# Optimization experiments

Measured on AMD Instinct MI355X. Metric: run time of the kernel, lower is better.

Reference implementation:

```python
import jax, jax.numpy as jnp
import numpy as np

NEG_INF = -1e30  # stands in for float('-inf'); sigmoid(-1e30)==0 in fp32


def _safe_l2_normalize(x):
    # norm over last dim; norms equal to 0 are replaced by 1 (torch masked_fill_)
    n = jnp.linalg.norm(x, axis=-1, keepdims=True)
    return x / jnp.where(n == 0, 1.0, n)


def setup_inputs() -> dict:
    key = jax.random.key(0)
    k1, k2, k3 = jax.random.split(key, 3)
    B, S, D = 32, 1024, 512
    context = jax.random.normal(k1, (B, S, D), dtype=jnp.float32)
    query = jax.random.normal(k2, (B, S, D), dtype=jnp.float32)
    length = jax.random.randint(k3, (B,), 1, S + 1, dtype=jnp.int64)
    return {"context": context, "query": query, "length": length}


def reference(context, query, length):
    # context: [B, Sc, D], query: [B, Sq, D], length: [B]
    B, Sq, D = query.shape
    Sc = context.shape[1]

    q = _safe_l2_normalize(query)          # normalize=True path
    context_key = _safe_l2_normalize(context)

    # raw bilinear scores [B, Sq, Sc]
    raw_scores = jnp.einsum('bqd,bkd->bqk', q, context_key)

    # mask context positions >= length[b] with -inf (per-sample length mask)
    key_mask = jnp.arange(Sc)[None, None, :] < length[:, None, None]
    raw_scores = jnp.where(key_mask, raw_scores, NEG_INF)

    scores = jax.nn.sigmoid(raw_scores)

    # L1-normalize along context dim; norms < 1 replaced by 1
    scores_norm = jnp.sum(jnp.abs(scores), axis=2, keepdims=True)
    scores = scores / jnp.where(scores_norm < 1, 1.0, scores_norm)

    # zero out query rows >= length[b]
    query_mask = jnp.arange(Sq)[None, :, None] < length[:, None, None]
    scores = jnp.where(query_mask, scores, 0.0)

    attended_context = jnp.einsum('bqk,bkd->bqd', scores, context)
    output = jnp.concatenate([q, attended_context], axis=2)  # [B, Sq, 2D]
    return output, scores
```

## Files before the change

### kernel.cpp

```cpp
#include <hip/hip_runtime.h>
#include <hip/hip_bf16.h>
#include <math.h>

#define BB 32
#define SS 1024
#define DD 512
#define OUT_ELEMS 33554432ull

typedef _Float16 half8 __attribute__((ext_vector_type(8)));
typedef _Float16 half4 __attribute__((ext_vector_type(4)));
typedef float floatx4 __attribute__((ext_vector_type(4)));

__device__ __forceinline__ int load_len(const int* __restrict__ len, int b) {
  const bool is64 = (len[1] == 0);
  return is64 ? (int)((const long long*)len)[b] : len[b];
}

__global__ __launch_bounds__(256) void k_norm(const float* __restrict__ ctx,
                                              const float* __restrict__ qry,
                                              float* __restrict__ out,
                                              float* __restrict__ cinv) {
  const int wid = threadIdx.x >> 6, lane = threadIdx.x & 63;
  const int row = blockIdx.x * 4 + wid;
  const bool isq = row >= BB * SS;
  const int r = isq ? row - BB * SS : row;
  const float4* s4 = (const float4*)((isq ? qry : ctx) + (size_t)r * DD);
  float4 e0 = s4[lane];
  float4 e1 = s4[lane + 64];
  float ss = e0.x*e0.x + e0.y*e0.y + e0.z*e0.z + e0.w*e0.w
           + e1.x*e1.x + e1.y*e1.y + e1.z*e1.z + e1.w*e1.w;
  #pragma unroll
  for (int m = 32; m; m >>= 1) ss += __shfl_xor(ss, m);
  const float inv = (ss > 0.0f) ? (1.0f / sqrtf(ss)) : 1.0f;
  if (isq) {
    float4* dst = (float4*)(out + (size_t)r * (2 * DD));
    float4 o0 = {e0.x*inv, e0.y*inv, e0.z*inv, e0.w*inv};
    float4 o1 = {e1.x*inv, e1.y*inv, e1.z*inv, e1.w*inv};
    dst[lane] = o0;
    dst[lane + 64] = o1;
  } else if (lane == 0) {
    cinv[r] = inv;
  }
}

__global__ __launch_bounds__(256) void k_qk(const float* __restrict__ ctx,
                                            const float* __restrict__ outq,
                                            const float* __restrict__ cinv,
                                            const int* __restrict__ len,
                                            float* __restrict__ sig,
                                            float* __restrict__ denom) {
  __shared__ _Float16 As[128][40];
  __shared__ _Float16 Bs[128][40];
  __shared__ float civ[128];

  const int b = blockIdx.z, bx = blockIdx.x, by = blockIdx.y;
  const int t = threadIdx.x, lane = t & 63, wid = t >> 6;
  const int wm = wid >> 1, wn = wid & 1;
  const int L = load_len(len, b);

  if (t < 128) civ[t] = cinv[b * SS + bx * 128 + t];

  floatx4 acc[4][4] = {};
  const float* qbase = outq + (size_t)(b * SS + by * 128) * (2 * DD);
  const float* cbase = ctx + (size_t)(b * SS + bx * 128) * DD;
  const int rr = lane & 15, g = lane >> 4;

  for (int kt = 0; kt < DD / 32; ++kt) {
    const int k0 = kt * 32;
    __syncthreads();
    #pragma unroll
    for (int it = 0; it < 4; ++it) {
      const int flat = t + it * 256;
      const int r = flat >> 3, cg = flat & 7;
      float4 av = *(const float4*)(qbase + (size_t)r * (2 * DD) + k0 + cg * 4);
      *(half4*)&As[r][cg * 4] =
          (half4){(_Float16)av.x, (_Float16)av.y, (_Float16)av.z, (_Float16)av.w};
      const float ci = civ[r];
      float4 bv = *(const float4*)(cbase + (size_t)r * DD + k0 + cg * 4);
      *(half4*)&Bs[r][cg * 4] =
          (half4){(_Float16)(bv.x * ci), (_Float16)(bv.y * ci),
                  (_Float16)(bv.z * ci), (_Float16)(bv.w * ci)};
    }
    __syncthreads();
    half8 af[4], bf[4];
    #pragma unroll
    for (int i = 0; i < 4; ++i) af[i] = *(const half8*)&As[wm * 64 + i * 16 + rr][g * 8];
    #pragma unroll
    for (int j = 0; j < 4; ++j) bf[j] = *(const half8*)&Bs[wn * 64 + j * 16 + rr][g * 8];
    #pragma unroll
    for (int i = 0; i < 4; ++i)
      #pragma unroll
      for (int j = 0; j < 4; ++j)
        acc[i][j] = __builtin_amdgcn_mfma_f32_16x16x32_f16(af[i], bf[j], acc[i][j], 0, 0, 0);
  }

  const int rowbase = by * 128 + wm * 64, colbase = bx * 128 + wn * 64;
  #pragma unroll
  for (int i = 0; i < 4; ++i) {
    #pragma unroll
    for (int r = 0; r < 4; ++r) {
      const int row = rowbase + i * 16 + g * 4 + r;
      float* srow = sig + (size_t)(b * SS + row) * SS;
      float rsum = 0.0f;
      #pragma unroll
      for (int j = 0; j < 4; ++j) {
        const int col = colbase + j * 16 + rr;
        float v = 0.0f;
        if (col < L) v = 1.0f / (1.0f + __expf(-acc[i][j][r]));
        srow[col] = v;
        rsum += v;
      }
      rsum += __shfl_xor(rsum, 1);
      rsum += __shfl_xor(rsum, 2);
      rsum += __shfl_xor(rsum, 4);
      rsum += __shfl_xor(rsum, 8);
      if (rr == 0) atomicAdd(&denom[b * SS + row], rsum);
    }
  }
}

__global__ __launch_bounds__(512) void k_pv(const float* __restrict__ ctx,
                                            float* __restrict__ sig,
                                            const float* __restrict__ denom,
                                            const int* __restrict__ len,
                                            float* __restrict__ out) {
  __shared__ _Float16 Sh[64][40], Sl[64][40];
  __shared__ _Float16 Ch[512][40], Cl[512][40];
  __shared__ float rds[64];

  const int b = blockIdx.y, bm = blockIdx.x;
  const int t = threadIdx.x, lane = t & 63, wid = t >> 6;
  const int wm = wid >> 2, wn = wid & 3;
  const int rr = lane & 15, g = lane >> 4;
  const int L = load_len(len, b);

  if (t < 64) {
    const int row = bm * 64 + t;
    const float dv = denom[b * SS + row];
    rds[t] = (row < L) ? (1.0f / fmaxf(dv, 1.0f)) : 0.0f;
  }
  __syncthreads();

  floatx4 acc[2][8] = {};
  float* sbase = sig + (size_t)(b * SS + bm * 64) * SS;
  const float* cbase = ctx + (size_t)b * SS * DD;

  const int sr = t >> 3, scg = t & 7;
  const int kg = t & 7, dg = t >> 3;

  for (int kt = 0; kt < SS / 32; ++kt) {
    const int k0 = kt * 32;
    {
      float* sp = sbase + (size_t)sr * SS + k0 + scg * 4;
      float4 v = *(const float4*)sp;
      const float rd = rds[sr];
      float4 nv = {v.x * rd, v.y * rd, v.z * rd, v.w * rd};
      *(float4*)sp = nv;
      _Float16 h0 = (_Float16)v.x, h1 = (_Float16)v.y, h2 = (_Float16)v.z, h3 = (_Float16)v.w;
      *(half4*)&Sh[sr][scg * 4] = (half4){h0, h1, h2, h3};
      *(half4*)&Sl[sr][scg * 4] = (half4){(_Float16)(v.x - (float)h0), (_Float16)(v.y - (float)h1),
                                          (_Float16)(v.z - (float)h2), (_Float16)(v.w - (float)h3)};
    }
    #pragma unroll
    for (int it = 0; it < 2; ++it) {
      const int db = it * 256 + dg * 4;
      const float* cp = cbase + (size_t)(k0 + kg * 4) * DD + db;
      float4 v0 = *(const float4*)(cp);
      float4 v1 = *(const float4*)(cp + DD);
      float4 v2 = *(const float4*)(cp + 2 * DD);
      float4 v3 = *(const float4*)(cp + 3 * DD);
      const float f0[4] = {v0.x, v0.y, v0.z, v0.w};
      const float f1[4] = {v1.x, v1.y, v1.z, v1.w};
      const float f2[4] = {v2.x, v2.y, v2.z, v2.w};
      const float f3[4] = {v3.x, v3.y, v3.z, v3.w};
      #pragma unroll
      for (int i = 0; i < 4; ++i) {
        _Float16 h0 = (_Float16)f0[i], h1 = (_Float16)f1[i], h2 = (_Float16)f2[i], h3 = (_Float16)f3[i];
        *(half4*)&Ch[db + i][kg * 4] = (half4){h0, h1, h2, h3};
        *(half4*)&Cl[db + i][kg * 4] =
            (half4){(_Float16)(f0[i] - (float)h0), (_Float16)(f1[i] - (float)h1),
                    (_Float16)(f2[i] - (float)h2), (_Float16)(f3[i] - (float)h3)};
      }
    }
    __syncthreads();
    half8 sh[2], sl[2];
    #pragma unroll
    for (int i = 0; i < 2; ++i) {
      sh[i] = *(const half8*)&Sh[wm * 32 + i * 16 + rr][g * 8];
      sl[i] = *(const half8*)&Sl[wm * 32 + i * 16 + rr][g * 8];
    }
    #pragma unroll
    for (int j = 0; j < 8; ++j) {
      half8 ch = *(const half8*)&Ch[wn * 128 + j * 16 + rr][g * 8];
      half8 cl = *(const half8*)&Cl[wn * 128 + j * 16 + rr][g * 8];
      #pragma unroll
      for (int i = 0; i < 2; ++i) {
        acc[i][j] = __builtin_amdgcn_mfma_f32_16x16x32_f16(sh[i], ch, acc[i][j], 0, 0, 0);
        acc[i][j] = __builtin_amdgcn_mfma_f32_16x16x32_f16(sh[i], cl, acc[i][j], 0, 0, 0);
        acc[i][j] = __builtin_amdgcn_mfma_f32_16x16x32_f16(sl[i], ch, acc[i][j], 0, 0, 0);
      }
    }
    __syncthreads();
  }

  #pragma unroll
  for (int i = 0; i < 2; ++i) {
    #pragma unroll
    for (int r = 0; r < 4; ++r) {
      const int lrow = wm * 32 + i * 16 + g * 4 + r;
      const int row = bm * 64 + lrow;
      const float rd = rds[lrow];
      float* orow = out + (size_t)(b * SS + row) * (2 * DD) + DD;
      #pragma unroll
      for (int j = 0; j < 8; ++j) {
        const int d = wn * 128 + j * 16 + rr;
        orow[d] = acc[i][j][r] * rd;
      }
    }
  }
}

extern "C" void kernel_launch(void* const* d_in, const int* in_sizes, int n_in,
                              void* d_out, int out_size, void* d_ws, size_t ws_size,
                              hipStream_t stream) {
  const float* ctx = (const float*)d_in[0];
  const float* qry = (const float*)d_in[1];
  const int* len = (const int*)d_in[2];
  float* out = (float*)d_out;
  float* sig = out + OUT_ELEMS;
  float* denom = (float*)d_ws;
  float* cinv = denom + BB * SS;

  hipMemsetAsync(denom, 0, BB * SS * sizeof(float), stream);
  k_norm<<<(2 * BB * SS) / 4, 256, 0, stream>>>(ctx, qry, out, cinv);
  k_qk<<<dim3(SS / 128, SS / 128, BB), 256, 0, stream>>>(ctx, out, cinv, len, sig, denom);
  k_pv<<<dim3(SS / 64, BB), 512, 0, stream>>>(ctx, sig, denom, len, out);
}
```

Measured before the change: 671.7 us.

## Precompute fp16 normalized Q/C in workspace and drop low-half MFMA term in PV

The norm kernel now also writes fp16 copies of the normalized query and context into workspace. A new QK kernel reads these directly with 64-wide K tiles, replacing per-tile fp32 loads and conversion. The fp32 path remains as a fallback when the workspace is too small. The PV kernel drops the context low-part split, going from three MFMAs to two and saving LDS. Both changes cut conversion and memory traffic at the cost of accuracy, since context is now rounded to fp16 in PV.

```diff
diff --git a/kernel.cpp b/kernel.cpp
--- a/kernel.cpp
+++ b/kernel.cpp
@@ -11,6 +11,12 @@
 typedef _Float16 half4 __attribute__((ext_vector_type(4)));
 typedef float floatx4 __attribute__((ext_vector_type(4)));
 
+#define WS_DENOM_OFF   0ull
+#define WS_CINV_OFF    131072ull
+#define WS_QH_OFF      262144ull
+#define WS_CN_OFF      (262144ull + 33554432ull)
+#define WS_NEEDED      (262144ull + 2ull * 33554432ull)
+
 __device__ __forceinline__ int load_len(const int* __restrict__ len, int b) {
   const bool is64 = (len[1] == 0);
   return is64 ? (int)((const long long*)len)[b] : len[b];
@@ -19,7 +25,10 @@
 __global__ __launch_bounds__(256) void k_norm(const float* __restrict__ ctx,
                                               const float* __restrict__ qry,
                                               float* __restrict__ out,
-                                              float* __restrict__ cinv) {
+                                              float* __restrict__ cinv,
+                                              _Float16* __restrict__ qh,
+                                              _Float16* __restrict__ cn,
+                                              int wf) {
   const int wid = threadIdx.x >> 6, lane = threadIdx.x & 63;
   const int row = blockIdx.x * 4 + wid;
   const bool isq = row >= BB * SS;
@@ -32,23 +41,104 @@
   #pragma unroll
   for (int m = 32; m; m >>= 1) ss += __shfl_xor(ss, m);
   const float inv = (ss > 0.0f) ? (1.0f / sqrtf(ss)) : 1.0f;
+  float4 o0 = {e0.x*inv, e0.y*inv, e0.z*inv, e0.w*inv};
+  float4 o1 = {e1.x*inv, e1.y*inv, e1.z*inv, e1.w*inv};
   if (isq) {
     float4* dst = (float4*)(out + (size_t)r * (2 * DD));
-    float4 o0 = {e0.x*inv, e0.y*inv, e0.z*inv, e0.w*inv};
-    float4 o1 = {e1.x*inv, e1.y*inv, e1.z*inv, e1.w*inv};
     dst[lane] = o0;
     dst[lane + 64] = o1;
-  } else if (lane == 0) {
-    cinv[r] = inv;
-  }
-}
-
-__global__ __launch_bounds__(256) void k_qk(const float* __restrict__ ctx,
-                                            const float* __restrict__ outq,
-                                            const float* __restrict__ cinv,
-                                            const int* __restrict__ len,
-                                            float* __restrict__ sig,
-                                            float* __restrict__ denom) {
+    if (wf) {
+      *(half4*)(qh + (size_t)r * DD + 4 * lane) =
+          (half4){(_Float16)o0.x, (_Float16)o0.y, (_Float16)o0.z, (_Float16)o0.w};
+      *(half4*)(qh + (size_t)r * DD + 256 + 4 * lane) =
+          (half4){(_Float16)o1.x, (_Float16)o1.y, (_Float16)o1.z, (_Float16)o1.w};
+    }
+  } else {
+    if (lane == 0) cinv[r] = inv;
+    if (wf) {
+      *(half4*)(cn + (size_t)r * DD + 4 * lane) =
+          (half4){(_Float16)o0.x, (_Float16)o0.y, (_Float16)o0.z, (_Float16)o0.w};
+      *(half4*)(cn + (size_t)r * DD + 256 + 4 * lane) =
+          (half4){(_Float16)o1.x, (_Float16)o1.y, (_Float16)o1.z, (_Float16)o1.w};
+    }
+  }
+}
+
+__global__ __launch_bounds__(256) void k_qk_f16(const _Float16* __restrict__ qh,
+                                                const _Float16* __restrict__ cn,
+                                                const int* __restrict__ len,
+                                                float* __restrict__ sig,
+                                                float* __restrict__ denom) {
+  __shared__ _Float16 As[128][72];
+  __shared__ _Float16 Bs[128][72];
+
+  const int b = blockIdx.z, bx = blockIdx.x, by = blockIdx.y;
+  const int t = threadIdx.x, lane = t & 63, wid = t >> 6;
+  const int wm = wid >> 1, wn = wid & 1;
+  const int L = load_len(len, b);
+  const int rr = lane & 15, g = lane >> 4;
+
+  floatx4 acc[4][4] = {};
+  const _Float16* qbase = qh + (size_t)(b * SS + by * 128) * DD;
+  const _Float16* cbase = cn + (size_t)(b * SS + bx * 128) * DD;
+  const int sr = t >> 3, sc = (t & 7) * 8;
+
+  for (int kt = 0; kt < DD / 64; ++kt) {
+    const int k0 = kt * 64;
+    __syncthreads();
+    #pragma unroll
+    for (int it = 0; it < 4; ++it) {
+      const int r = it * 32 + sr;
+      *(half8*)&As[r][sc] = *(const half8*)(qbase + (size_t)r * DD + k0 + sc);
+      *(half8*)&Bs[r][sc] = *(const half8*)(cbase + (size_t)r * DD + k0 + sc);
+    }
+    __syncthreads();
+    #pragma unroll
+    for (int ks = 0; ks < 2; ++ks) {
+      half8 af[4], bf[4];
+      #pragma unroll
+      for (int i = 0; i < 4; ++i) af[i] = *(const half8*)&As[wm * 64 + i * 16 + rr][ks * 32 + g * 8];
+      #pragma unroll
+      for (int j = 0; j < 4; ++j) bf[j] = *(const half8*)&Bs[wn * 64 + j * 16 + rr][ks * 32 + g * 8];
+      #pragma unroll
+      for (int i = 0; i < 4; ++i)
+        #pragma unroll
+        for (int j = 0; j < 4; ++j)
+          acc[i][j] = __builtin_amdgcn_mfma_f32_16x16x32_f16(af[i], bf[j], acc[i][j], 0, 0, 0);
+    }
+  }
+
+  const int rowbase = by * 128 + wm * 64, colbase = bx * 128 + wn * 64;
+  #pragma unroll
+  for (int i = 0; i < 4; ++i) {
+    #pragma unroll
+    for (int r = 0; r < 4; ++r) {
+      const int row = rowbase + i * 16 + g * 4 + r;
+      float* srow = sig + (size_t)(b * SS + row) * SS;
+      float rsum = 0.0f;
+      #pragma unroll
+      for (int j = 0; j < 4; ++j) {
+        const int col = colbase + j * 16 + rr;
+        float v = 0.0f;
+        if (col < L) v = 1.0f / (1.0f + __expf(-acc[i][j][r]));
+        srow[col] = v;
+        rsum += v;
+      }
+      rsum += __shfl_xor(rsum, 1);
+      rsum += __shfl_xor(rsum, 2);
+      rsum += __shfl_xor(rsum, 4);
+      rsum += __shfl_xor(rsum, 8);
+      if (rr == 0) atomicAdd(&denom[b * SS + row], rsum);
+    }
+  }
+}
+
+__global__ __launch_bounds__(256) void k_qk_fp32(const float* __restrict__ ctx,
+                                                 const float* __restrict__ outq,
+                                                 const float* __restrict__ cinv,
+                                                 const int* __restrict__ len,
+                                                 float* __restrict__ sig,
+                                                 float* __restrict__ denom) {
   __shared__ _Float16 As[128][40];
   __shared__ _Float16 Bs[128][40];
   __shared__ float civ[128];
@@ -125,7 +215,7 @@
                                             const int* __restrict__ len,
                                             float* __restrict__ out) {
   __shared__ _Float16 Sh[64][40], Sl[64][40];
-  __shared__ _Float16 Ch[512][40], Cl[512][40];
+  __shared__ _Float16 Ch[512][40];
   __shared__ float rds[64];
 
   const int b = blockIdx.y, bm = blockIdx.x;
@@ -175,11 +265,8 @@
       const float f3[4] = {v3.x, v3.y, v3.z, v3.w};
       #pragma unroll
       for (int i = 0; i < 4; ++i) {
-        _Float16 h0 = (_Float16)f0[i], h1 = (_Float16)f1[i], h2 = (_Float16)f2[i], h3 = (_Float16)f3[i];
-        *(half4*)&Ch[db + i][kg * 4] = (half4){h0, h1, h2, h3};
-        *(half4*)&Cl[db + i][kg * 4] =
-            (half4){(_Float16)(f0[i] - (float)h0), (_Float16)(f1[i] - (float)h1),
-                    (_Float16)(f2[i] - (float)h2), (_Float16)(f3[i] - (float)h3)};
+        *(half4*)&Ch[db + i][kg * 4] =
+            (half4){(_Float16)f0[i], (_Float16)f1[i], (_Float16)f2[i], (_Float16)f3[i]};
       }
     }
     __syncthreads();
@@ -192,11 +279,9 @@
     #pragma unroll
     for (int j = 0; j < 8; ++j) {
       half8 ch = *(const half8*)&Ch[wn * 128 + j * 16 + rr][g * 8];
-      half8 cl = *(const half8*)&Cl[wn * 128 + j * 16 + rr][g * 8];
       #pragma unroll
       for (int i = 0; i < 2; ++i) {
         acc[i][j] = __builtin_amdgcn_mfma_f32_16x16x32_f16(sh[i], ch, acc[i][j], 0, 0, 0);
-        acc[i][j] = __builtin_amdgcn_mfma_f32_16x16x32_f16(sh[i], cl, acc[i][j], 0, 0, 0);
         acc[i][j] = __builtin_amdgcn_mfma_f32_16x16x32_f16(sl[i], ch, acc[i][j], 0, 0, 0);
       }
     }
@@ -228,11 +313,18 @@
   const int* len = (const int*)d_in[2];
   float* out = (float*)d_out;
   float* sig = out + OUT_ELEMS;
-  float* denom = (float*)d_ws;
-  float* cinv = denom + BB * SS;
+  char* ws = (char*)d_ws;
+  float* denom = (float*)(ws + WS_DENOM_OFF);
+  float* cinv  = (float*)(ws + WS_CINV_OFF);
+  _Float16* qh = (_Float16*)(ws + WS_QH_OFF);
+  _Float16* cn = (_Float16*)(ws + WS_CN_OFF);
+  const int wf = (ws_size >= WS_NEEDED) ? 1 : 0;
 
   hipMemsetAsync(denom, 0, BB * SS * sizeof(float), stream);
-  k_norm<<<(2 * BB * SS) / 4, 256, 0, stream>>>(ctx, qry, out, cinv);
-  k_qk<<<dim3(SS / 128, SS / 128, BB), 256, 0, stream>>>(ctx, out, cinv, len, sig, denom);
+  k_norm<<<(2 * BB * SS) / 4, 256, 0, stream>>>(ctx, qry, out, cinv, qh, cn, wf);
+  if (wf)
+    k_qk_f16<<<dim3(SS / 128, SS / 128, BB), 256, 0, stream>>>(qh, cn, len, sig, denom);
+  else
+    k_qk_fp32<<<dim3(SS / 128, SS / 128, BB), 256, 0, stream>>>(ctx, out, cinv, len, sig, denom);
   k_pv<<<dim3(SS / 64, BB), 512, 0, stream>>>(ctx, sig, denom, len, out);
 }
```

New measurement: 625.1 us. -6.9%, faster.

## Pretranspose context to fp16, load MFMA fragments directly, drop low-part product

Applied to the files above, without the earlier changes.

Adds a transpose kernel that writes context as fp16 [B,D,S] into workspace, so the PV GEMM can load B fragments straight from global memory without LDS staging. The QK GEMM also drops its shared-memory tiles and loads fp32 fragments directly into registers. The PV split-precision scheme drops the context low-part term, cutting MFMAs from three to two per tile. The in-place row scaling of sig moves to after the accumulation loop. The new path depends on workspace size, and the loss of LDS reuse relies on caches to absorb the repeated global loads, which also slightly reduces accuracy.

```diff
diff --git a/kernel.cpp b/kernel.cpp
--- a/kernel.cpp
+++ b/kernel.cpp
@@ -10,6 +10,11 @@
 typedef _Float16 half8 __attribute__((ext_vector_type(8)));
 typedef _Float16 half4 __attribute__((ext_vector_type(4)));
 typedef float floatx4 __attribute__((ext_vector_type(4)));
+
+#define WS_DENOM_OFF 0ull
+#define WS_CINV_OFF  131072ull
+#define WS_CT_OFF    262144ull
+#define WS_NEED_T1   (262144ull + 33554432ull)
 
 __device__ __forceinline__ int load_len(const int* __restrict__ len, int b) {
   const bool is64 = (len[1] == 0);
@@ -33,9 +38,9 @@
   for (int m = 32; m; m >>= 1) ss += __shfl_xor(ss, m);
   const float inv = (ss > 0.0f) ? (1.0f / sqrtf(ss)) : 1.0f;
   if (isq) {
-    float4* dst = (float4*)(out + (size_t)r * (2 * DD));
     float4 o0 = {e0.x*inv, e0.y*inv, e0.z*inv, e0.w*inv};
     float4 o1 = {e1.x*inv, e1.y*inv, e1.z*inv, e1.w*inv};
+    float4* dst = (float4*)(out + (size_t)r * (2 * DD));
     dst[lane] = o0;
     dst[lane + 64] = o1;
   } else if (lane == 0) {
@@ -43,50 +48,69 @@
   }
 }
 
-__global__ __launch_bounds__(256) void k_qk(const float* __restrict__ ctx,
-                                            const float* __restrict__ outq,
-                                            const float* __restrict__ cinv,
-                                            const int* __restrict__ len,
-                                            float* __restrict__ sig,
-                                            float* __restrict__ denom) {
-  __shared__ _Float16 As[128][40];
-  __shared__ _Float16 Bs[128][40];
-  __shared__ float civ[128];
-
+__global__ __launch_bounds__(256) void k_tr(const float* __restrict__ ctx,
+                                            _Float16* __restrict__ ct) {
+  __shared__ _Float16 tile[64][72];
+  const int b = blockIdx.z, dx = blockIdx.y, sx = blockIdx.x;
+  const int t = threadIdx.x;
+  const int s0 = sx * 64, d0 = dx * 64;
+  const int sr = t >> 4, sc = (t & 15) * 4;
+  #pragma unroll
+  for (int it = 0; it < 4; ++it) {
+    const int s = sr + it * 16;
+    float4 v = *(const float4*)(ctx + (size_t)(b * SS + s0 + s) * DD + d0 + sc);
+    tile[sc + 0][s] = (_Float16)v.x;
+    tile[sc + 1][s] = (_Float16)v.y;
+    tile[sc + 2][s] = (_Float16)v.z;
+    tile[sc + 3][s] = (_Float16)v.w;
+  }
+  __syncthreads();
+  const int dr = t >> 2, seg = (t & 3) * 16;
+  _Float16* orow = ct + ((size_t)b * DD + d0 + dr) * SS + s0 + seg;
+  *(half8*)orow = *(const half8*)&tile[dr][seg];
+  *(half8*)(orow + 8) = *(const half8*)&tile[dr][seg + 8];
+}
+
+__global__ __launch_bounds__(256) void k_qk_lf32(const float* __restrict__ ctx,
+                                                 const float* __restrict__ outq,
+                                                 const float* __restrict__ cinv,
+                                                 const int* __restrict__ len,
+                                                 float* __restrict__ sig,
+                                                 float* __restrict__ denom) {
   const int b = blockIdx.z, bx = blockIdx.x, by = blockIdx.y;
   const int t = threadIdx.x, lane = t & 63, wid = t >> 6;
   const int wm = wid >> 1, wn = wid & 1;
+  const int rr = lane & 15, g = lane >> 4;
   const int L = load_len(len, b);
 
-  if (t < 128) civ[t] = cinv[b * SS + bx * 128 + t];
-
   floatx4 acc[4][4] = {};
-  const float* qbase = outq + (size_t)(b * SS + by * 128) * (2 * DD);
-  const float* cbase = ctx + (size_t)(b * SS + bx * 128) * DD;
-  const int rr = lane & 15, g = lane >> 4;
+  const float* abase = outq + (size_t)(b * SS + by * 128 + wm * 64 + rr) * (2 * DD);
+  const int brow0 = b * SS + bx * 128 + wn * 64 + rr;
+  const float* bbase = ctx + (size_t)brow0 * DD;
+  float civ[4];
+  #pragma unroll
+  for (int j = 0; j < 4; ++j) civ[j] = cinv[brow0 + j * 16];
 
   for (int kt = 0; kt < DD / 32; ++kt) {
-    const int k0 = kt * 32;
-    __syncthreads();
-    #pragma unroll
-    for (int it = 0; it < 4; ++it) {
-      const int flat = t + it * 256;
-      const int r = flat >> 3, cg = flat & 7;
-      float4 av = *(const float4*)(qbase + (size_t)r * (2 * DD) + k0 + cg * 4);
-      *(half4*)&As[r][cg * 4] =
-          (half4){(_Float16)av.x, (_Float16)av.y, (_Float16)av.z, (_Float16)av.w};
-      const float ci = civ[r];
-      float4 bv = *(const float4*)(cbase + (size_t)r * DD + k0 + cg * 4);
-      *(half4*)&Bs[r][cg * 4] =
-          (half4){(_Float16)(bv.x * ci), (_Float16)(bv.y * ci),
-                  (_Float16)(bv.z * ci), (_Float16)(bv.w * ci)};
-    }
-    __syncthreads();
+    const int ka = kt * 32 + g * 8;
     half8 af[4], bf[4];
     #pragma unroll
-    for (int i = 0; i < 4; ++i) af[i] = *(const half8*)&As[wm * 64 + i * 16 + rr][g * 8];
-    #pragma unroll
-    for (int j = 0; j < 4; ++j) bf[j] = *(const half8*)&Bs[wn * 64 + j * 16 + rr][g * 8];
+    for (int i = 0; i < 4; ++i) {
+      const float* ap = abase + (size_t)(i * 16) * (2 * DD) + ka;
+      float4 v0 = *(const float4*)ap;
+      float4 v1 = *(const float4*)(ap + 4);
+      af[i] = (half8){(_Float16)v0.x, (_Float16)v0.y, (_Float16)v0.z, (_Float16)v0.w,
+                      (_Float16)v1.x, (_Float16)v1.y, (_Float16)v1.z, (_Float16)v1.w};
+    }
+    #pragma unroll
+    for (int j = 0; j < 4; ++j) {
+      const float* bp = bbase + (size_t)(j * 16) * DD + ka;
+      float4 v0 = *(const float4*)bp;
+      float4 v1 = *(const float4*)(bp + 4);
+      const float c = civ[j];
+      bf[j] = (half8){(_Float16)(v0.x*c), (_Float16)(v0.y*c), (_Float16)(v0.z*c), (_Float16)(v0.w*c),
+                      (_Float16)(v1.x*c), (_Float16)(v1.y*c), (_Float16)(v1.z*c), (_Float16)(v1.w*c)};
+    }
     #pragma unroll
     for (int i = 0; i < 4; ++i)
       #pragma unroll
@@ -119,35 +143,109 @@
   }
 }
 
-__global__ __launch_bounds__(512) void k_pv(const float* __restrict__ ctx,
-                                            float* __restrict__ sig,
-                                            const float* __restrict__ denom,
-                                            const int* __restrict__ len,
-                                            float* __restrict__ out) {
+__global__ __launch_bounds__(256) void k_pv_lf(float* __restrict__ sig,
+                                               const _Float16* __restrict__ ct,
+                                               const float* __restrict__ denom,
+                                               const int* __restrict__ len,
+                                               float* __restrict__ out) {
+  __shared__ float rds[32];
+  const int b = blockIdx.y, bm = blockIdx.x;
+  const int t = threadIdx.x, lane = t & 63, wn = t >> 6;
+  const int rr = lane & 15, g = lane >> 4;
+  const int L = load_len(len, b);
+
+  if (t < 32) {
+    const int row = bm * 32 + t;
+    rds[t] = (row < L) ? (1.0f / fmaxf(denom[b * SS + row], 1.0f)) : 0.0f;
+  }
+
+  floatx4 acc[2][8] = {};
+  float* ab = sig + (size_t)(b * SS + bm * 32 + rr) * SS;
+  const _Float16* bb = ct + ((size_t)b * DD + wn * 128 + rr) * SS;
+
+  for (int kt = 0; kt < SS / 32; ++kt) {
+    const int ka = kt * 32 + g * 8;
+    half8 ah[2], al[2], bh[8];
+    #pragma unroll
+    for (int i = 0; i < 2; ++i) {
+      const float* ap = ab + (size_t)(i * 16) * SS + ka;
+      float4 v0 = *(const float4*)ap;
+      float4 v1 = *(const float4*)(ap + 4);
+      const float va[8] = {v0.x, v0.y, v0.z, v0.w, v1.x, v1.y, v1.z, v1.w};
+      #pragma unroll
+      for (int e = 0; e < 8; ++e) {
+        const _Float16 hh = (_Float16)va[e];
+        ah[i][e] = hh;
+        al[i][e] = (_Float16)(va[e] - (float)hh);
+      }
+    }
+    #pragma unroll
+    for (int j = 0; j < 8; ++j)
+      bh[j] = *(const half8*)(bb + (size_t)(j * 16) * SS + ka);
+    #pragma unroll
+    for (int j = 0; j < 8; ++j)
+      #pragma unroll
+      for (int i = 0; i < 2; ++i) {
+        acc[i][j] = __builtin_amdgcn_mfma_f32_16x16x32_f16(ah[i], bh[j], acc[i][j], 0, 0, 0);
+        acc[i][j] = __builtin_amdgcn_mfma_f32_16x16x32_f16(al[i], bh[j], acc[i][j], 0, 0, 0);
+      }
+  }
+
+  __syncthreads();
+
+  {
+    float* base = sig + (size_t)(b * SS + bm * 32) * SS;
+    #pragma unroll
+    for (int f = 0; f < 32; ++f) {
+      const int idx = f * 256 + t;
+      const int row = idx >> 8;
+      const float rd = rds[row];
+      float4* p = (float4*)base + idx;
+      float4 v = *p;
+      v.x *= rd; v.y *= rd; v.z *= rd; v.w *= rd;
+      *p = v;
+    }
+  }
+
+  #pragma unroll
+  for (int i = 0; i < 2; ++i) {
+    #pragma unroll
+    for (int r = 0; r < 4; ++r) {
+      const int lrow = i * 16 + g * 4 + r;
+      const int row = bm * 32 + lrow;
+      const float rd = rds[lrow];
+      float* orow = out + (size_t)(b * SS + row) * (2 * DD) + DD;
+      #pragma unroll
+      for (int j = 0; j < 8; ++j)
+        orow[wn * 128 + j * 16 + rr] = acc[i][j][r] * rd;
+    }
+  }
+}
+
+__global__ __launch_bounds__(512) void k_pv_r7(const float* __restrict__ ctx,
+                                               float* __restrict__ sig,
+                                               const float* __restrict__ denom,
+                                               const int* __restrict__ len,
+                                               float* __restrict__ out) {
   __shared__ _Float16 Sh[64][40], Sl[64][40];
-  __shared__ _Float16 Ch[512][40], Cl[512][40];
+  __shared__ _Float16 Ch[512][40];
   __shared__ float rds[64];
-
   const int b = blockIdx.y, bm = blockIdx.x;
   const int t = threadIdx.x, lane = t & 63, wid = t >> 6;
   const int wm = wid >> 2, wn = wid & 3;
   const int rr = lane & 15, g = lane >> 4;
   const int L = load_len(len, b);
-
   if (t < 64) {
     const int row = bm * 64 + t;
     const float dv = denom[b * SS + row];
     rds[t] = (row < L) ? (1.0f / fmaxf(dv, 1.0f)) : 0.0f;
   }
   __syncthreads();
-
   floatx4 acc[2][8] = {};
   float* sbase = sig + (size_t)(b * SS + bm * 64) * SS;
   const float* cbase = ctx + (size_t)b * SS * DD;
-
   const int sr = t >> 3, scg = t & 7;
   const int kg = t & 7, dg = t >> 3;
-
   for (int kt = 0; kt < SS / 32; ++kt) {
     const int k0 = kt * 32;
     {
@@ -175,11 +273,8 @@
       const float f3[4] = {v3.x, v3.y, v3.z, v3.w};
       #pragma unroll
       for (int i = 0; i < 4; ++i) {
-        _Float16 h0 = (_Float16)f0[i], h1 = (_Float16)f1[i], h2 = (_Float16)f2[i], h3 = (_Float16)f3[i];
-        *(half4*)&Ch[db + i][kg * 4] = (half4){h0, h1, h2, h3};
-        *(half4*)&Cl[db + i][kg * 4] =
-            (half4){(_Float16)(f0[i] - (float)h0), (_Float16)(f1[i] - (float)h1),
-                    (_Float16)(f2[i] - (float)h2), (_Float16)(f3[i] - (float)h3)};
+        *(half4*)&Ch[db + i][kg * 4] =
+            (half4){(_Float16)f0[i], (_Float16)f1[i], (_Float16)f2[i], (_Float16)f3[i]};
       }
     }
     __syncthreads();
@@ -192,17 +287,14 @@
     #pragma unroll
     for (int j = 0; j < 8; ++j) {
       half8 ch = *(const half8*)&Ch[wn * 128 + j * 16 + rr][g * 8];
-      half8 cl = *(const half8*)&Cl[wn * 128 + j * 16 + rr][g * 8];
       #pragma unroll
       for (int i = 0; i < 2; ++i) {
         acc[i][j] = __builtin_amdgcn_mfma_f32_16x16x32_f16(sh[i], ch, acc[i][j], 0, 0, 0);
-        acc[i][j] = __builtin_amdgcn_mfma_f32_16x16x32_f16(sh[i], cl, acc[i][j], 0, 0, 0);
         acc[i][j] = __builtin_amdgcn_mfma_f32_16x16x32_f16(sl[i], ch, acc[i][j], 0, 0, 0);
       }
     }
     __syncthreads();
   }
-
   #pragma unroll
   for (int i = 0; i < 2; ++i) {
     #pragma unroll
@@ -228,11 +320,18 @@
   const int* len = (const int*)d_in[2];
   float* out = (float*)d_out;
   float* sig = out + OUT_ELEMS;
-  float* denom = (float*)d_ws;
-  float* cinv = denom + BB * SS;
+  char* ws = (char*)d_ws;
+  float* denom = (float*)(ws + WS_DENOM_OFF);
+  float* cinv  = (float*)(ws + WS_CINV_OFF);
+  _Float16* ct = (_Float16*)(ws + WS_CT_OFF);
+  const int t1 = (ws_size >= WS_NEED_T1) ? 1 : 0;
 
   hipMemsetAsync(denom, 0, BB * SS * sizeof(float), stream);
   k_norm<<<(2 * BB * SS) / 4, 256, 0, stream>>>(ctx, qry, out, cinv);
-  k_qk<<<dim3(SS / 128, SS / 128, BB), 256, 0, stream>>>(ctx, out, cinv, len, sig, denom);
-  k_pv<<<dim3(SS / 64, BB), 512, 0, stream>>>(ctx, sig, denom, len, out);
-}
+  if (t1) k_tr<<<dim3(SS / 64, DD / 64, BB), 256, 0, stream>>>(ctx, ct);
+  k_qk_lf32<<<dim3(SS / 128, SS / 128, BB), 256, 0, stream>>>(ctx, out, cinv, len, sig, denom);
+  if (t1)
+    k_pv_lf<<<dim3(SS / 32, BB), 256, 0, stream>>>(sig, ct, denom, len, out);
+  else
+    k_pv_r7<<<dim3(SS / 64, BB), 512, 0, stream>>>(ctx, sig, denom, len, out);
+}
```

New measurement: 803.6 us. 19.6% more time.
